# Optimization experiments

Hardware: AMD Instinct MI355X
Metric: run time of the kernel (lower is better)

The kernel has to match this reference:

```python
import jax, jax.numpy as jnp
import numpy as np

N_NODES = 50000
N_EDGES = 800000
D_HIDDEN = 128
N_LAYERS = 3


def setup_inputs() -> dict:
    key = jax.random.key(0)
    k1, k2, k3 = jax.random.split(key, 3)
    x = jax.random.normal(k1, (N_NODES, D_HIDDEN), dtype=jnp.float32)
    edge_index = jax.random.randint(k2, (2, N_EDGES), 0, N_NODES, dtype=jnp.int32)
    # per-layer GCNConv params: weight [d,d], bias [d] (PyG lin has bias merged into conv bias)
    Ws = jax.random.normal(k3, (N_LAYERS, D_HIDDEN, D_HIDDEN), dtype=jnp.float32) / np.sqrt(D_HIDDEN).astype(np.float32)
    bs = jnp.zeros((N_LAYERS, D_HIDDEN), dtype=jnp.float32)
    return {"x": x, "edge_index": edge_index, "Ws": Ws, "bs": bs}


def reference(x, edge_index, Ws, bs):
    n = x.shape[0]
    # PyG GCNConv default: add self-loops, symmetric degree normalization.
    loops = jnp.arange(n, dtype=edge_index.dtype)
    src = jnp.concatenate([edge_index[0], loops])  # message sources (x_j)
    dst = jnp.concatenate([edge_index[1], loops])  # aggregation targets
    deg = jax.ops.segment_sum(jnp.ones_like(src, dtype=x.dtype), dst, num_segments=n)
    dinv = jnp.where(deg > 0, jax.lax.rsqrt(deg), jnp.zeros_like(deg))
    norm = dinv[src] * dinv[dst]  # [E+N]; edge_index is static across layers so compute once
    for l in range(Ws.shape[0]):
        h = x @ Ws[l]                                  # dense linear [N, d]
        msg = h[src] * norm[:, None]                   # gather + normalize [E+N, d]
        x = jax.ops.segment_sum(msg, dst, num_segments=n) + bs[l]  # scatter-add
    # single GELU applied after the final layer (per the original forward)
    x = jax.nn.gelu(x, approximate=False)
    return x
```

## Files before the change

### kernel.cpp

```cpp
#include <hip/hip_runtime.h>
#include <math.h>

#define D 128

typedef __attribute__((ext_vector_type(8))) short short8v;
typedef __attribute__((ext_vector_type(4))) float f32x4;

__device__ __forceinline__ unsigned short f2bf(float x) {
    unsigned int u = __float_as_uint(x);
    unsigned int r = (u + 0x7FFFu + ((u >> 16) & 1u)) >> 16;
    return (unsigned short)r;
}
__device__ __forceinline__ float bf2f(unsigned short b) {
    return __uint_as_float(((unsigned int)b) << 16);
}


__global__ void zero_k(int* __restrict__ cnt, int n) {
    int i = blockIdx.x * blockDim.x + threadIdx.x;
    if (i < n) cnt[i] = 0;
}

__global__ void rank_k(const int* __restrict__ dst, int E,
                       int* __restrict__ cnt, unsigned short* __restrict__ rank) {
    int e = blockIdx.x * blockDim.x + threadIdx.x;
    if (e < E) rank[e] = (unsigned short)atomicAdd(&cnt[dst[e]], 1);
}

__global__ __launch_bounds__(1024) void scan_a(const int* __restrict__ cnt, int N,
                                               int* __restrict__ part, int* __restrict__ bsum) {
    __shared__ int s[1024];
    int i = blockIdx.x * 1024 + threadIdx.x;
    int v = (i < N) ? cnt[i] : 0;
    s[threadIdx.x] = v;
    __syncthreads();
    for (int off = 1; off < 1024; off <<= 1) {
        int add = (threadIdx.x >= off) ? s[threadIdx.x - off] : 0;
        __syncthreads();
        s[threadIdx.x] += add;
        __syncthreads();
    }
    if (i < N) part[i] = s[threadIdx.x] - v;
    if (threadIdx.x == 1023) bsum[blockIdx.x] = s[1023];
}

__global__ __launch_bounds__(1024) void scan_b(int* __restrict__ bsum, int nb) {
    __shared__ int s[1024];
    int v = (threadIdx.x < nb) ? bsum[threadIdx.x] : 0;
    s[threadIdx.x] = v;
    __syncthreads();
    for (int off = 1; off < 1024; off <<= 1) {
        int add = (threadIdx.x >= off) ? s[threadIdx.x - off] : 0;
        __syncthreads();
        s[threadIdx.x] += add;
        __syncthreads();
    }
    if (threadIdx.x < nb) bsum[threadIdx.x] = s[threadIdx.x] - v;
}

__global__ void scan_c(const int* __restrict__ cnt, int* __restrict__ part,
                       const int* __restrict__ bsum,
                       float* __restrict__ dinv, int N, int E) {
    int i = blockIdx.x * blockDim.x + threadIdx.x;
    if (i < N) {
        part[i] = part[i] + bsum[i >> 10];
        dinv[i] = rsqrtf((float)(cnt[i] + 1));
    }
    if (i == 0) part[N] = E;
}

__global__ void fill_k(const int* __restrict__ src, const int* __restrict__ dst,
                       const unsigned short* __restrict__ rank, const int* __restrict__ rp,
                       int E, unsigned short* __restrict__ ssrc) {
    int e = blockIdx.x * blockDim.x + threadIdx.x;
    if (e < E) {
        int p = rp[dst[e]] + (int)rank[e];
        ssrc[p] = (unsigned short)src[e];
    }
}


__global__ void wsplit_k(const float* __restrict__ Wp, short* __restrict__ BFh,
                         short* __restrict__ BFl, int total) {
    int idx = blockIdx.x * blockDim.x + threadIdx.x;
    if (idx >= total) return;
    int i    = idx & 7;
    int lane = (idx >> 3) & 63;
    int ct   = (idx >> 9) & 7;
    int ks   = (idx >> 12) & 3;
    int l    = idx >> 14;
    int k = ks * 32 + (lane >> 4) * 8 + i;
    int n = ct * 16 + (lane & 15);
    float w = Wp[(size_t)l * (D * D) + (size_t)k * D + n];
    unsigned short h = f2bf(w);
    float lo = w - bf2f(h);
    BFh[idx] = (short)h;
    BFl[idx] = (short)f2bf(lo);
}


__global__ __launch_bounds__(256) void gemm_k(const float* __restrict__ X,
                                              const short* __restrict__ BFh,
                                              const short* __restrict__ BFl,
                                              const float* __restrict__ dinv,
                                              unsigned short* __restrict__ Hb, int M) {
    int lane = threadIdx.x & 63;
    int wv = threadIdx.x >> 6;
    int rowBase = blockIdx.x * 64 + wv * 16;
    int arow = rowBase + (lane & 15);
    bool aval = arow < M;
    const float* xr = X + (size_t)arow * D + (lane >> 4) * 8;

    short8v ah[4], al[4];
#pragma unroll
    for (int ks = 0; ks < 4; ++ks) {
        float4 p = make_float4(0.f, 0.f, 0.f, 0.f);
        float4 q = make_float4(0.f, 0.f, 0.f, 0.f);
        if (aval) {
            p = *(const float4*)(xr + ks * 32);
            q = *(const float4*)(xr + ks * 32 + 4);
        }
        float v[8] = {p.x, p.y, p.z, p.w, q.x, q.y, q.z, q.w};
#pragma unroll
        for (int i = 0; i < 8; ++i) {
            unsigned short h = f2bf(v[i]);
            ah[ks][i] = (short)h;
            al[ks][i] = (short)f2bf(v[i] - bf2f(h));
        }
    }

    int rb = rowBase + (lane >> 4) * 4;
    float dsc[4];
#pragma unroll
    for (int i = 0; i < 4; ++i) dsc[i] = (rb + i < M) ? dinv[rb + i] : 0.f;

    const short8v* Bh = (const short8v*)BFh;
    const short8v* Bl = (const short8v*)BFl;
#pragma unroll
    for (int ct = 0; ct < 8; ++ct) {
        short8v bh[4], bl[4];
#pragma unroll
        for (int ks = 0; ks < 4; ++ks) {
            bh[ks] = Bh[(ks * 8 + ct) * 64 + lane];
            bl[ks] = Bl[(ks * 8 + ct) * 64 + lane];
        }
        f32x4 acc = {0.f, 0.f, 0.f, 0.f};
#pragma unroll
        for (int ks = 0; ks < 4; ++ks) {
            acc = __builtin_amdgcn_mfma_f32_16x16x32_bf16(ah[ks], bh[ks], acc, 0, 0, 0);
            acc = __builtin_amdgcn_mfma_f32_16x16x32_bf16(al[ks], bh[ks], acc, 0, 0, 0);
            acc = __builtin_amdgcn_mfma_f32_16x16x32_bf16(ah[ks], bl[ks], acc, 0, 0, 0);
        }
        int c = ct * 16 + (lane & 15);
#pragma unroll
        for (int i = 0; i < 4; ++i) {
            int r = rb + i;
            if (r < M) Hb[(size_t)r * D + c] = f2bf(dsc[i] * acc[i]);
        }
    }
}


__device__ __forceinline__ float gelu_f(float x) {
    return 0.5f * x * (1.0f + erff(x * 0.70710678118654752f));
}

__global__ __launch_bounds__(256) void agg_k(const unsigned short* __restrict__ Hb,
                                             const int* __restrict__ rp,
                                             const unsigned short* __restrict__ ssrc,
                                             const float* __restrict__ dinv,
                                             const float* __restrict__ bias,
                                             float* __restrict__ out, int N, int doGelu) {
    int node = blockIdx.x * 4 + (threadIdx.x >> 6);
    int lane = threadIdx.x & 63;
    if (node >= N) return;
    const unsigned int* __restrict__ hb = (const unsigned int*)Hb;
    unsigned int sv = hb[(size_t)node * 64 + lane];
    float ax = __uint_as_float(sv << 16);
    float ay = __uint_as_float(sv & 0xFFFF0000u);
    float bx = 0.f, by = 0.f;
    int e0 = rp[node];
    int e1 = rp[node + 1];
    for (int base = e0; base < e1; base += 64) {
        int idxv = 0;
        if (base + lane < e1) idxv = (int)ssrc[base + lane];
        int cnt = e1 - base; if (cnt > 64) cnt = 64;
        for (int c = 0; c < cnt; c += 16) {
            int s[16];
            unsigned int v[16];
#pragma unroll
            for (int j = 0; j < 16; ++j) s[j] = __shfl(idxv, c + j);
#pragma unroll
            for (int j = 0; j < 16; ++j) v[j] = hb[(size_t)s[j] * 64 + lane];
#pragma unroll
            for (int j = 0; j < 16; ++j) {
                unsigned int m = (c + j < cnt) ? v[j] : 0u;
                float fx = __uint_as_float(m << 16);
                float fy = __uint_as_float(m & 0xFFFF0000u);
                if (j & 1) { bx += fx; by += fy; }
                else       { ax += fx; ay += fy; }
            }
        }
    }
    ax += bx; ay += by;
    float dn = dinv[node];
    float2 bv = ((const float2*)bias)[lane];
    ax = dn * ax + bv.x;
    ay = dn * ay + bv.y;
    if (doGelu) { ax = gelu_f(ax); ay = gelu_f(ay); }
    ((float2*)out)[(size_t)node * 64 + lane] = make_float2(ax, ay);
}


extern "C" void kernel_launch(void* const* d_in, const int* in_sizes, int n_in,
                              void* d_out, int out_size, void* d_ws, size_t ws_size,
                              hipStream_t stream) {
    const float* X  = (const float*)d_in[0];
    const int*   EI = (const int*)d_in[1];
    const float* Wp = (const float*)d_in[2];
    const float* bp = (const float*)d_in[3];
    float* OUT = (float*)d_out;

    int N = in_sizes[0] / D;
    int E = in_sizes[1] / 2;
    int L = in_sizes[3] / D;
    const int* src = EI;
    const int* dst = EI + E;

    char* w = (char*)d_ws;
    auto alloc = [&](size_t bytes) {
        char* p = w;
        w += (bytes + 255) & ~(size_t)255;
        return p;
    };
    unsigned short* HB = (unsigned short*)alloc((size_t)N * D * sizeof(unsigned short));
    float* XB   = (float*)alloc((size_t)N * D * sizeof(float));
    float* DINV = (float*)alloc((size_t)N * sizeof(float));
    int*   RP   = (int*)alloc((size_t)(N + 1) * sizeof(int));
    int*   CNT  = (int*)alloc((size_t)N * sizeof(int));
    int*   BSUM = (int*)alloc(4096 * sizeof(int));
    unsigned short* RANK = (unsigned short*)alloc((size_t)E * sizeof(unsigned short));
    unsigned short* SSRC = (unsigned short*)alloc(((size_t)E + 64) * sizeof(unsigned short));
    short* BFH  = (short*)alloc((size_t)L * D * D * sizeof(short));
    short* BFL  = (short*)alloc((size_t)L * D * D * sizeof(short));
    (void)ws_size; (void)n_in; (void)out_size;

    zero_k<<<(N + 255) / 256, 256, 0, stream>>>(CNT, N);

    int eb = (E + 255) / 256;
    rank_k<<<eb, 256, 0, stream>>>(dst, E, CNT, RANK);
    int nb = (N + 1023) / 1024;
    scan_a<<<nb, 1024, 0, stream>>>(CNT, N, RP, BSUM);
    scan_b<<<1, 1024, 0, stream>>>(BSUM, nb);
    scan_c<<<(N + 255) / 256, 256, 0, stream>>>(CNT, RP, BSUM, DINV, N, E);
    fill_k<<<eb, 256, 0, stream>>>(src, dst, RANK, RP, E, SSRC);

    int wtot = L * D * D;
    wsplit_k<<<(wtot + 255) / 256, 256, 0, stream>>>(Wp, BFH, BFL, wtot);

    int gb = (N + 63) / 64;
    int ab = (N + 3) / 4;
    for (int l = 0; l < L; ++l) {
        const float* xin = (l == 0) ? X : XB;
        gemm_k<<<gb, 256, 0, stream>>>(xin, BFH + (size_t)l * D * D, BFL + (size_t)l * D * D,
                                       DINV, HB, N);
        float* o = (l == L - 1) ? OUT : XB;
        agg_k<<<ab, 256, 0, stream>>>(HB, RP, SSRC, DINV, bp + (size_t)l * D, o, N,
                                      (l == L - 1) ? 1 : 0);
    }
}
```

Baseline: 212.1 us.

## Vectorize aggregation gathers to 16-byte rows and fold block-sum scan into scan_c

```diff
diff --git a/kernel.cpp b/kernel.cpp
--- a/kernel.cpp
+++ b/kernel.cpp
@@ -44,26 +44,21 @@
     if (threadIdx.x == 1023) bsum[blockIdx.x] = s[1023];
 }
 
-__global__ __launch_bounds__(1024) void scan_b(int* __restrict__ bsum, int nb) {
-    __shared__ int s[1024];
-    int v = (threadIdx.x < nb) ? bsum[threadIdx.x] : 0;
-    s[threadIdx.x] = v;
+__global__ __launch_bounds__(256) void scan_c(const int* __restrict__ cnt, int* __restrict__ part,
+                                              const int* __restrict__ bsum,
+                                              float* __restrict__ dinv, int N, int E) {
+    __shared__ int s_pref;
+    int chunk = blockIdx.x >> 2;
+    if (threadIdx.x < 64) {
+        int v = (threadIdx.x < chunk) ? bsum[threadIdx.x] : 0;
+#pragma unroll
+        for (int off = 1; off < 64; off <<= 1) v += __shfl_xor(v, off);
+        if (threadIdx.x == 0) s_pref = v;
+    }
     __syncthreads();
-    for (int off = 1; off < 1024; off <<= 1) {
-        int add = (threadIdx.x >= off) ? s[threadIdx.x - off] : 0;
-        __syncthreads();
-        s[threadIdx.x] += add;
-        __syncthreads();
-    }
-    if (threadIdx.x < nb) bsum[threadIdx.x] = s[threadIdx.x] - v;
-}
-
-__global__ void scan_c(const int* __restrict__ cnt, int* __restrict__ part,
-                       const int* __restrict__ bsum,
-                       float* __restrict__ dinv, int N, int E) {
     int i = blockIdx.x * blockDim.x + threadIdx.x;
     if (i < N) {
-        part[i] = part[i] + bsum[i >> 10];
+        part[i] = part[i] + s_pref;
         dinv[i] = rsqrtf((float)(cnt[i] + 1));
     }
     if (i == 0) part[N] = E;
@@ -174,11 +169,14 @@
     int node = blockIdx.x * 4 + (threadIdx.x >> 6);
     int lane = threadIdx.x & 63;
     if (node >= N) return;
-    const unsigned int* __restrict__ hb = (const unsigned int*)Hb;
-    unsigned int sv = hb[(size_t)node * 64 + lane];
-    float ax = __uint_as_float(sv << 16);
-    float ay = __uint_as_float(sv & 0xFFFF0000u);
-    float bx = 0.f, by = 0.f;
+    const uint4* __restrict__ hb4 = (const uint4*)Hb;
+    int grp = lane >> 4;
+    int sub = lane & 15;
+
+    float acc[8];
+#pragma unroll
+    for (int i = 0; i < 8; ++i) acc[i] = 0.f;
+
     int e0 = rp[node];
     int e1 = rp[node + 1];
     for (int base = e0; base < e1; base += 64) {
@@ -186,29 +184,55 @@
         if (base + lane < e1) idxv = (int)ssrc[base + lane];
         int cnt = e1 - base; if (cnt > 64) cnt = 64;
         for (int c = 0; c < cnt; c += 16) {
-            int s[16];
-            unsigned int v[16];
-#pragma unroll
-            for (int j = 0; j < 16; ++j) s[j] = __shfl(idxv, c + j);
-#pragma unroll
-            for (int j = 0; j < 16; ++j) v[j] = hb[(size_t)s[j] * 64 + lane];
-#pragma unroll
-            for (int j = 0; j < 16; ++j) {
-                unsigned int m = (c + j < cnt) ? v[j] : 0u;
-                float fx = __uint_as_float(m << 16);
-                float fy = __uint_as_float(m & 0xFFFF0000u);
-                if (j & 1) { bx += fx; by += fy; }
-                else       { ax += fx; ay += fy; }
+            uint4 v[4];
+#pragma unroll
+            for (int j = 0; j < 4; ++j) {
+                int row = __shfl(idxv, c + 4 * j + grp);
+                v[j] = hb4[(size_t)row * 16 + sub];
             }
-        }
-    }
-    ax += bx; ay += by;
-    float dn = dinv[node];
-    float2 bv = ((const float2*)bias)[lane];
-    ax = dn * ax + bv.x;
-    ay = dn * ay + bv.y;
-    if (doGelu) { ax = gelu_f(ax); ay = gelu_f(ay); }
-    ((float2*)out)[(size_t)node * 64 + lane] = make_float2(ax, ay);
+#pragma unroll
+            for (int j = 0; j < 4; ++j) {
+                bool ok = (base + c + 4 * j + grp) < e1;
+                unsigned int w;
+                w = ok ? v[j].x : 0u;
+                acc[0] += __uint_as_float(w << 16); acc[1] += __uint_as_float(w & 0xFFFF0000u);
+                w = ok ? v[j].y : 0u;
+                acc[2] += __uint_as_float(w << 16); acc[3] += __uint_as_float(w & 0xFFFF0000u);
+                w = ok ? v[j].z : 0u;
+                acc[4] += __uint_as_float(w << 16); acc[5] += __uint_as_float(w & 0xFFFF0000u);
+                w = ok ? v[j].w : 0u;
+                acc[6] += __uint_as_float(w << 16); acc[7] += __uint_as_float(w & 0xFFFF0000u);
+            }
+        }
+    }
+#pragma unroll
+    for (int i = 0; i < 8; ++i) {
+        acc[i] += __shfl_xor(acc[i], 16);
+        acc[i] += __shfl_xor(acc[i], 32);
+    }
+    if (lane < 16) {
+        uint4 sv = hb4[(size_t)node * 16 + lane];
+        acc[0] += __uint_as_float(sv.x << 16); acc[1] += __uint_as_float(sv.x & 0xFFFF0000u);
+        acc[2] += __uint_as_float(sv.y << 16); acc[3] += __uint_as_float(sv.y & 0xFFFF0000u);
+        acc[4] += __uint_as_float(sv.z << 16); acc[5] += __uint_as_float(sv.z & 0xFFFF0000u);
+        acc[6] += __uint_as_float(sv.w << 16); acc[7] += __uint_as_float(sv.w & 0xFFFF0000u);
+        float dn = dinv[node];
+        float4 b0 = ((const float4*)bias)[lane * 2];
+        float4 b1 = ((const float4*)bias)[lane * 2 + 1];
+        float r[8];
+        r[0] = dn * acc[0] + b0.x; r[1] = dn * acc[1] + b0.y;
+        r[2] = dn * acc[2] + b0.z; r[3] = dn * acc[3] + b0.w;
+        r[4] = dn * acc[4] + b1.x; r[5] = dn * acc[5] + b1.y;
+        r[6] = dn * acc[6] + b1.z; r[7] = dn * acc[7] + b1.w;
+        if (doGelu) {
+#pragma unroll
+            for (int i = 0; i < 8; ++i) r[i] = gelu_f(r[i]);
+        }
+        float4 o0 = make_float4(r[0], r[1], r[2], r[3]);
+        float4 o1 = make_float4(r[4], r[5], r[6], r[7]);
+        ((float4*)out)[(size_t)node * 32 + lane * 2]     = o0;
+        ((float4*)out)[(size_t)node * 32 + lane * 2 + 1] = o1;
+    }
 }
 
 
@@ -251,7 +275,6 @@
     rank_k<<<eb, 256, 0, stream>>>(dst, E, CNT, RANK);
     int nb = (N + 1023) / 1024;
     scan_a<<<nb, 1024, 0, stream>>>(CNT, N, RP, BSUM);
-    scan_b<<<1, 1024, 0, stream>>>(BSUM, nb);
     scan_c<<<(N + 255) / 256, 256, 0, stream>>>(CNT, RP, BSUM, DINV, N, E);
     fill_k<<<eb, 256, 0, stream>>>(src, dst, RANK, RP, E, SSRC);
 
```

After: 210.8 us. No clear change (-0.6%).

## Slice hidden features into 16-column panels and aggregate per slice; fold block-sum scan

Applied to the files above, without the earlier changes.

```diff
diff --git a/kernel.cpp b/kernel.cpp
--- a/kernel.cpp
+++ b/kernel.cpp
@@ -44,26 +44,21 @@
     if (threadIdx.x == 1023) bsum[blockIdx.x] = s[1023];
 }
 
-__global__ __launch_bounds__(1024) void scan_b(int* __restrict__ bsum, int nb) {
-    __shared__ int s[1024];
-    int v = (threadIdx.x < nb) ? bsum[threadIdx.x] : 0;
-    s[threadIdx.x] = v;
+__global__ __launch_bounds__(256) void scan_c(const int* __restrict__ cnt, int* __restrict__ part,
+                                              const int* __restrict__ bsum,
+                                              float* __restrict__ dinv, int N, int E) {
+    __shared__ int s_pref;
+    int chunk = blockIdx.x >> 2;
+    if (threadIdx.x < 64) {
+        int v = (threadIdx.x < chunk) ? bsum[threadIdx.x] : 0;
+#pragma unroll
+        for (int off = 1; off < 64; off <<= 1) v += __shfl_xor(v, off);
+        if (threadIdx.x == 0) s_pref = v;
+    }
     __syncthreads();
-    for (int off = 1; off < 1024; off <<= 1) {
-        int add = (threadIdx.x >= off) ? s[threadIdx.x - off] : 0;
-        __syncthreads();
-        s[threadIdx.x] += add;
-        __syncthreads();
-    }
-    if (threadIdx.x < nb) bsum[threadIdx.x] = s[threadIdx.x] - v;
-}
-
-__global__ void scan_c(const int* __restrict__ cnt, int* __restrict__ part,
-                       const int* __restrict__ bsum,
-                       float* __restrict__ dinv, int N, int E) {
     int i = blockIdx.x * blockDim.x + threadIdx.x;
     if (i < N) {
-        part[i] = part[i] + bsum[i >> 10];
+        part[i] = part[i] + s_pref;
         dinv[i] = rsqrtf((float)(cnt[i] + 1));
     }
     if (i == 0) part[N] = E;
@@ -103,7 +98,7 @@
                                               const short* __restrict__ BFh,
                                               const short* __restrict__ BFl,
                                               const float* __restrict__ dinv,
-                                              unsigned short* __restrict__ Hb, int M) {
+                                              unsigned short* __restrict__ HS, int M) {
     int lane = threadIdx.x & 63;
     int wv = threadIdx.x >> 6;
     int rowBase = blockIdx.x * 64 + wv * 16;
@@ -151,11 +146,10 @@
             acc = __builtin_amdgcn_mfma_f32_16x16x32_bf16(al[ks], bh[ks], acc, 0, 0, 0);
             acc = __builtin_amdgcn_mfma_f32_16x16x32_bf16(ah[ks], bl[ks], acc, 0, 0, 0);
         }
-        int c = ct * 16 + (lane & 15);
 #pragma unroll
         for (int i = 0; i < 4; ++i) {
             int r = rb + i;
-            if (r < M) Hb[(size_t)r * D + c] = f2bf(dsc[i] * acc[i]);
+            if (r < M) HS[((size_t)ct * M + r) * 16 + (lane & 15)] = f2bf(dsc[i] * acc[i]);
         }
     }
 }
@@ -165,20 +159,20 @@
     return 0.5f * x * (1.0f + erff(x * 0.70710678118654752f));
 }
 
-__global__ __launch_bounds__(256) void agg_k(const unsigned short* __restrict__ Hb,
+__global__ __launch_bounds__(256) void agg_k(const unsigned short* __restrict__ HS,
                                              const int* __restrict__ rp,
                                              const unsigned short* __restrict__ ssrc,
                                              const float* __restrict__ dinv,
                                              const float* __restrict__ bias,
                                              float* __restrict__ out, int N, int doGelu) {
-    int node = blockIdx.x * 4 + (threadIdx.x >> 6);
-    int lane = threadIdx.x & 63;
+    int slice = blockIdx.x & 7;
+    int node  = (blockIdx.x >> 3) * 4 + (threadIdx.x >> 6);
+    int lane  = threadIdx.x & 63;
     if (node >= N) return;
-    const unsigned int* __restrict__ hb = (const unsigned int*)Hb;
-    unsigned int sv = hb[(size_t)node * 64 + lane];
-    float ax = __uint_as_float(sv << 16);
-    float ay = __uint_as_float(sv & 0xFFFF0000u);
-    float bx = 0.f, by = 0.f;
+    int g = lane >> 2, sub = lane & 3;
+    const uint2* __restrict__ hs = (const uint2*)(HS + (size_t)slice * N * 16);
+
+    float a0 = 0.f, a1 = 0.f, a2 = 0.f, a3 = 0.f;
     int e0 = rp[node];
     int e1 = rp[node + 1];
     for (int base = e0; base < e1; base += 64) {
@@ -186,29 +180,36 @@
         if (base + lane < e1) idxv = (int)ssrc[base + lane];
         int cnt = e1 - base; if (cnt > 64) cnt = 64;
         for (int c = 0; c < cnt; c += 16) {
-            int s[16];
-            unsigned int v[16];
-#pragma unroll
-            for (int j = 0; j < 16; ++j) s[j] = __shfl(idxv, c + j);
-#pragma unroll
-            for (int j = 0; j < 16; ++j) v[j] = hb[(size_t)s[j] * 64 + lane];
-#pragma unroll
-            for (int j = 0; j < 16; ++j) {
-                unsigned int m = (c + j < cnt) ? v[j] : 0u;
-                float fx = __uint_as_float(m << 16);
-                float fy = __uint_as_float(m & 0xFFFF0000u);
-                if (j & 1) { bx += fx; by += fy; }
-                else       { ax += fx; ay += fy; }
-            }
-        }
-    }
-    ax += bx; ay += by;
-    float dn = dinv[node];
-    float2 bv = ((const float2*)bias)[lane];
-    ax = dn * ax + bv.x;
-    ay = dn * ay + bv.y;
-    if (doGelu) { ax = gelu_f(ax); ay = gelu_f(ay); }
-    ((float2*)out)[(size_t)node * 64 + lane] = make_float2(ax, ay);
+            int row = __shfl(idxv, c + g);
+            uint2 v = hs[(size_t)row * 4 + sub];
+            bool ok = (base + c + g) < e1;
+            unsigned int w;
+            w = ok ? v.x : 0u;
+            a0 += __uint_as_float(w << 16); a1 += __uint_as_float(w & 0xFFFF0000u);
+            w = ok ? v.y : 0u;
+            a2 += __uint_as_float(w << 16); a3 += __uint_as_float(w & 0xFFFF0000u);
+        }
+    }
+#pragma unroll
+    for (int m = 4; m < 64; m <<= 1) {
+        a0 += __shfl_xor(a0, m);
+        a1 += __shfl_xor(a1, m);
+        a2 += __shfl_xor(a2, m);
+        a3 += __shfl_xor(a3, m);
+    }
+    if (g == 0) {
+        uint2 sv = hs[(size_t)node * 4 + sub];
+        a0 += __uint_as_float(sv.x << 16); a1 += __uint_as_float(sv.x & 0xFFFF0000u);
+        a2 += __uint_as_float(sv.y << 16); a3 += __uint_as_float(sv.y & 0xFFFF0000u);
+        float dn = dinv[node];
+        float4 bv = ((const float4*)bias)[slice * 4 + sub];
+        float r0 = dn * a0 + bv.x;
+        float r1 = dn * a1 + bv.y;
+        float r2 = dn * a2 + bv.z;
+        float r3 = dn * a3 + bv.w;
+        if (doGelu) { r0 = gelu_f(r0); r1 = gelu_f(r1); r2 = gelu_f(r2); r3 = gelu_f(r3); }
+        ((float4*)out)[(size_t)node * 32 + slice * 4 + sub] = make_float4(r0, r1, r2, r3);
+    }
 }
 
 
@@ -251,7 +252,6 @@
     rank_k<<<eb, 256, 0, stream>>>(dst, E, CNT, RANK);
     int nb = (N + 1023) / 1024;
     scan_a<<<nb, 1024, 0, stream>>>(CNT, N, RP, BSUM);
-    scan_b<<<1, 1024, 0, stream>>>(BSUM, nb);
     scan_c<<<(N + 255) / 256, 256, 0, stream>>>(CNT, RP, BSUM, DINV, N, E);
     fill_k<<<eb, 256, 0, stream>>>(src, dst, RANK, RP, E, SSRC);
 
@@ -259,7 +259,7 @@
     wsplit_k<<<(wtot + 255) / 256, 256, 0, stream>>>(Wp, BFH, BFL, wtot);
 
     int gb = (N + 63) / 64;
-    int ab = (N + 3) / 4;
+    int ab = ((N + 3) / 4) * 8;
     for (int l = 0; l < L; ++l) {
         const float* xin = (l == 0) ? X : XB;
         gemm_k<<<gb, 256, 0, stream>>>(xin, BFH + (size_t)l * D * D, BFL + (size_t)l * D * D,
```

After: 441.2 us. 108% more time.

## Merge setup kernels, fuse CSR fill with first GEMM, pipeline gather loads

Applied to the files above, without the earlier changes.

```diff
diff --git a/kernel.cpp b/kernel.cpp
--- a/kernel.cpp
+++ b/kernel.cpp
@@ -16,10 +16,26 @@
 }
 
 
-__global__ void zero_k(int* __restrict__ cnt, int n) {
-    int i = blockIdx.x * blockDim.x + threadIdx.x;
-    if (i < n) cnt[i] = 0;
-}
+__global__ void prep_k(const float* __restrict__ Wp, short* __restrict__ BFh,
+                       short* __restrict__ BFl, int wtot,
+                       int* __restrict__ cnt, int N) {
+    int idx = blockIdx.x * blockDim.x + threadIdx.x;
+    if (idx < wtot) {
+        int i    = idx & 7;
+        int lane = (idx >> 3) & 63;
+        int ct   = (idx >> 9) & 7;
+        int ks   = (idx >> 12) & 3;
+        int l    = idx >> 14;
+        int k = ks * 32 + (lane >> 4) * 8 + i;
+        int n = ct * 16 + (lane & 15);
+        float w = Wp[(size_t)l * (D * D) + (size_t)k * D + n];
+        unsigned short h = f2bf(w);
+        BFh[idx] = (short)h;
+        BFl[idx] = (short)f2bf(w - bf2f(h));
+    }
+    if (idx < N) cnt[idx] = 0;
+}
+
 
 __global__ void rank_k(const int* __restrict__ dst, int E,
                        int* __restrict__ cnt, unsigned short* __restrict__ rank) {
@@ -44,69 +60,36 @@
     if (threadIdx.x == 1023) bsum[blockIdx.x] = s[1023];
 }
 
-__global__ __launch_bounds__(1024) void scan_b(int* __restrict__ bsum, int nb) {
-    __shared__ int s[1024];
-    int v = (threadIdx.x < nb) ? bsum[threadIdx.x] : 0;
-    s[threadIdx.x] = v;
+__global__ __launch_bounds__(256) void scan_c(const int* __restrict__ cnt, int* __restrict__ part,
+                                              const int* __restrict__ bsum,
+                                              float* __restrict__ dinv, int N, int E) {
+    __shared__ int s_pref;
+    int chunk = blockIdx.x >> 2;
+    if (threadIdx.x < 64) {
+        int v = (threadIdx.x < chunk) ? bsum[threadIdx.x] : 0;
+#pragma unroll
+        for (int off = 1; off < 64; off <<= 1) v += __shfl_xor(v, off);
+        if (threadIdx.x == 0) s_pref = v;
+    }
     __syncthreads();
-    for (int off = 1; off < 1024; off <<= 1) {
-        int add = (threadIdx.x >= off) ? s[threadIdx.x - off] : 0;
-        __syncthreads();
-        s[threadIdx.x] += add;
-        __syncthreads();
-    }
-    if (threadIdx.x < nb) bsum[threadIdx.x] = s[threadIdx.x] - v;
-}
-
-__global__ void scan_c(const int* __restrict__ cnt, int* __restrict__ part,
-                       const int* __restrict__ bsum,
-                       float* __restrict__ dinv, int N, int E) {
     int i = blockIdx.x * blockDim.x + threadIdx.x;
     if (i < N) {
-        part[i] = part[i] + bsum[i >> 10];
+        part[i] = part[i] + s_pref;
         dinv[i] = rsqrtf((float)(cnt[i] + 1));
     }
     if (i == 0) part[N] = E;
 }
 
-__global__ void fill_k(const int* __restrict__ src, const int* __restrict__ dst,
-                       const unsigned short* __restrict__ rank, const int* __restrict__ rp,
-                       int E, unsigned short* __restrict__ ssrc) {
-    int e = blockIdx.x * blockDim.x + threadIdx.x;
-    if (e < E) {
-        int p = rp[dst[e]] + (int)rank[e];
-        ssrc[p] = (unsigned short)src[e];
-    }
-}
-
-
-__global__ void wsplit_k(const float* __restrict__ Wp, short* __restrict__ BFh,
-                         short* __restrict__ BFl, int total) {
-    int idx = blockIdx.x * blockDim.x + threadIdx.x;
-    if (idx >= total) return;
-    int i    = idx & 7;
-    int lane = (idx >> 3) & 63;
-    int ct   = (idx >> 9) & 7;
-    int ks   = (idx >> 12) & 3;
-    int l    = idx >> 14;
-    int k = ks * 32 + (lane >> 4) * 8 + i;
-    int n = ct * 16 + (lane & 15);
-    float w = Wp[(size_t)l * (D * D) + (size_t)k * D + n];
-    unsigned short h = f2bf(w);
-    float lo = w - bf2f(h);
-    BFh[idx] = (short)h;
-    BFl[idx] = (short)f2bf(lo);
-}
-
-
-__global__ __launch_bounds__(256) void gemm_k(const float* __restrict__ X,
-                                              const short* __restrict__ BFh,
-                                              const short* __restrict__ BFl,
-                                              const float* __restrict__ dinv,
-                                              unsigned short* __restrict__ Hb, int M) {
-    int lane = threadIdx.x & 63;
-    int wv = threadIdx.x >> 6;
-    int rowBase = blockIdx.x * 64 + wv * 16;
+
+__device__ __forceinline__ void gemm_body(const float* __restrict__ X,
+                                          const short* __restrict__ BFh,
+                                          const short* __restrict__ BFl,
+                                          const float* __restrict__ dinv,
+                                          unsigned short* __restrict__ Hb, int M,
+                                          int bid, int tid) {
+    int lane = tid & 63;
+    int wv = tid >> 6;
+    int rowBase = bid * 64 + wv * 16;
     int arow = rowBase + (lane & 15);
     bool aval = arow < M;
     const float* xr = X + (size_t)arow * D + (lane >> 4) * 8;
@@ -160,10 +143,54 @@
     }
 }
 
+__global__ __launch_bounds__(256) void gemm_k(const float* __restrict__ X,
+                                              const short* __restrict__ BFh,
+                                              const short* __restrict__ BFl,
+                                              const float* __restrict__ dinv,
+                                              unsigned short* __restrict__ Hb, int M) {
+    gemm_body(X, BFh, BFl, dinv, Hb, M, blockIdx.x, threadIdx.x);
+}
+
+__global__ __launch_bounds__(256) void fillgemm_k(const float* __restrict__ X,
+                                                  const short* __restrict__ BFh,
+                                                  const short* __restrict__ BFl,
+                                                  const float* __restrict__ dinv,
+                                                  unsigned short* __restrict__ Hb, int M, int gb,
+                                                  const int* __restrict__ src,
+                                                  const int* __restrict__ dst,
+                                                  const unsigned short* __restrict__ rank,
+                                                  const int* __restrict__ rp, int E,
+                                                  unsigned short* __restrict__ ssrc) {
+    if ((int)blockIdx.x < gb) {
+        gemm_body(X, BFh, BFl, dinv, Hb, M, blockIdx.x, threadIdx.x);
+    } else {
+        int e = (blockIdx.x - gb) * blockDim.x + threadIdx.x;
+        if (e < E) {
+            int p = rp[dst[e]] + (int)rank[e];
+            ssrc[p] = (unsigned short)src[e];
+        }
+    }
+}
+
 
 __device__ __forceinline__ float gelu_f(float x) {
     return 0.5f * x * (1.0f + erff(x * 0.70710678118654752f));
 }
+
+#define LOADR(V, C)                                                     \
+    _Pragma("unroll") for (int j = 0; j < 16; ++j) {                    \
+        int s_ = __shfl(idxv, (C) + j);                                 \
+        V[j] = hb[(size_t)s_ * 64 + lane];                              \
+    }
+
+#define CONSUME(V, C)                                                   \
+    _Pragma("unroll") for (int j = 0; j < 16; ++j) {                    \
+        unsigned int m_ = (base + (C) + j < e1) ? V[j] : 0u;            \
+        float fx_ = __uint_as_float(m_ << 16);                          \
+        float fy_ = __uint_as_float(m_ & 0xFFFF0000u);                  \
+        if (j & 1) { bx += fx_; by += fy_; }                            \
+        else       { ax += fx_; ay += fy_; }                            \
+    }
 
 __global__ __launch_bounds__(256) void agg_k(const unsigned short* __restrict__ Hb,
                                              const int* __restrict__ rp,
@@ -185,20 +212,17 @@
         int idxv = 0;
         if (base + lane < e1) idxv = (int)ssrc[base + lane];
         int cnt = e1 - base; if (cnt > 64) cnt = 64;
-        for (int c = 0; c < cnt; c += 16) {
-            int s[16];
-            unsigned int v[16];
-#pragma unroll
-            for (int j = 0; j < 16; ++j) s[j] = __shfl(idxv, c + j);
-#pragma unroll
-            for (int j = 0; j < 16; ++j) v[j] = hb[(size_t)s[j] * 64 + lane];
-#pragma unroll
-            for (int j = 0; j < 16; ++j) {
-                unsigned int m = (c + j < cnt) ? v[j] : 0u;
-                float fx = __uint_as_float(m << 16);
-                float fy = __uint_as_float(m & 0xFFFF0000u);
-                if (j & 1) { bx += fx; by += fy; }
-                else       { ax += fx; ay += fy; }
+        unsigned int vA[16], vB[16], vC[16];
+        LOADR(vA, 0);
+        if (cnt > 16) LOADR(vB, 16);
+        if (cnt > 32) LOADR(vC, 32);
+        CONSUME(vA, 0);
+        if (cnt > 16) {
+            if (cnt > 48) LOADR(vA, 48);
+            CONSUME(vB, 16);
+            if (cnt > 32) {
+                CONSUME(vC, 32);
+                if (cnt > 48) CONSUME(vA, 48);
             }
         }
     }
@@ -245,27 +269,26 @@
     short* BFL  = (short*)alloc((size_t)L * D * D * sizeof(short));
     (void)ws_size; (void)n_in; (void)out_size;
 
-    zero_k<<<(N + 255) / 256, 256, 0, stream>>>(CNT, N);
+    int wtot = L * D * D;
+    int pb = ((N > wtot ? N : wtot) + 255) / 256;
+    prep_k<<<pb, 256, 0, stream>>>(Wp, BFH, BFL, wtot, CNT, N);
 
     int eb = (E + 255) / 256;
     rank_k<<<eb, 256, 0, stream>>>(dst, E, CNT, RANK);
     int nb = (N + 1023) / 1024;
     scan_a<<<nb, 1024, 0, stream>>>(CNT, N, RP, BSUM);
-    scan_b<<<1, 1024, 0, stream>>>(BSUM, nb);
     scan_c<<<(N + 255) / 256, 256, 0, stream>>>(CNT, RP, BSUM, DINV, N, E);
-    fill_k<<<eb, 256, 0, stream>>>(src, dst, RANK, RP, E, SSRC);
-
-    int wtot = L * D * D;
-    wsplit_k<<<(wtot + 255) / 256, 256, 0, stream>>>(Wp, BFH, BFL, wtot);
 
     int gb = (N + 63) / 64;
+    fillgemm_k<<<gb + eb, 256, 0, stream>>>(X, BFH, BFL, DINV, HB, N, gb,
+                                            src, dst, RANK, RP, E, SSRC);
+
     int ab = (N + 3) / 4;
-    for (int l = 0; l < L; ++l) {
-        const float* xin = (l == 0) ? X : XB;
-        gemm_k<<<gb, 256, 0, stream>>>(xin, BFH + (size_t)l * D * D, BFL + (size_t)l * D * D,
-                                       DINV, HB, N);
-        float* o = (l == L - 1) ? OUT : XB;
-        agg_k<<<ab, 256, 0, stream>>>(HB, RP, SSRC, DINV, bp + (size_t)l * D, o, N,
-                                      (l == L - 1) ? 1 : 0);
-    }
-}
+    agg_k<<<ab, 256, 0, stream>>>(HB, RP, SSRC, DINV, bp, XB, N, 0);
+    gemm_k<<<gb, 256, 0, stream>>>(XB, BFH + (size_t)1 * D * D, BFL + (size_t)1 * D * D,
+                                   DINV, HB, N);
+    agg_k<<<ab, 256, 0, stream>>>(HB, RP, SSRC, DINV, bp + D, XB, N, 0);
+    gemm_k<<<gb, 256, 0, stream>>>(XB, BFH + (size_t)2 * D * D, BFL + (size_t)2 * D * D,
+                                   DINV, HB, N);
+    agg_k<<<ab, 256, 0, stream>>>(HB, RP, SSRC, DINV, bp + 2 * D, OUT, N, 1);
+}
```

New measurement: 258.9 us. +22.1%, slower.
